# Kernel tuning notes

Hardware: AMD Instinct MI355X
Metric: run time of the kernel (lower is better)

## Reference

```python
import jax, jax.numpy as jnp
import numpy as np

TIMESTEPS = 1000


def setup_inputs() -> dict:
    key = jax.random.key(0)
    k1, k2 = jax.random.split(key)
    rec = jax.random.uniform(k1, (64, 1, 256, 256), dtype=jnp.float32)
    tgt = jax.random.uniform(k2, (64, 1, 256, 256), dtype=jnp.float32)
    return {"reconstructed_image": rec, "target_image": tgt}


def _holographic_transform(img):
    # img: [B, 1, H, W] -> out: [B, 1, H, TIMESTEPS]
    # Original: for every nonzero pixel (x, y) with value v, writes
    #   out[b, 0, x, int(v * timesteps) - 1] = y
    # iterating in row-major (y ascending) order, so for duplicate targets the
    B, C, H, W = img.shape
    x = img[:, 0]  # [B, H, W]
    q = (x * TIMESTEPS).astype(jnp.int32) - 1
    # torch negative indexing wraps (q = -1 -> timesteps - 1); zero pixels are
    # skipped, so route them to an out-of-range index and drop.
    q = jnp.where(x != 0, q % TIMESTEPS, TIMESTEPS)  # [B, H, W]
    y_vals = jnp.broadcast_to(jnp.arange(W, dtype=img.dtype), (B, H, W))
    b_idx = jnp.arange(B)[:, None, None]
    h_idx = jnp.arange(H)[None, :, None]
    out = jnp.zeros((B, 1, H, TIMESTEPS), dtype=img.dtype)
    out = out.at[b_idx, 0, h_idx, q].max(y_vals, mode="drop")
    return out


def reference(reconstructed_image, target_image):
    rec_holo = _holographic_transform(reconstructed_image)
    tgt_holo = _holographic_transform(target_image)
    return jnp.mean((rec_holo - tgt_holo) ** 2)
```

## Files before the change

### kernel.cpp

```cpp
#include <hip/hip_runtime.h>

#define TIMESTEPS 1000
#define NROWS 16384
#define ROWS_PER_WAVE 4
#define WAVES_PER_BLOCK 4
#define NBLOCKS (NROWS / (ROWS_PER_WAVE * WAVES_PER_BLOCK))
#define NPARTIALS (NROWS / ROWS_PER_WAVE)
#define TOTAL_ELEMS 16384000.0

__global__ __launch_bounds__(256) void holo_row_loss(
    const float* __restrict__ rec,
    const float* __restrict__ tgt,
    float* __restrict__ partials)
{
    __shared__ int bins[WAVES_PER_BLOCK][2048];

    const int tid  = threadIdx.x;
    const int wav  = tid >> 6;
    const int lane = tid & 63;
    const int gw   = blockIdx.x * WAVES_PER_BLOCK + wav;

    int* __restrict__ binw = &bins[wav][0];

    int4 z4; z4.x = 0; z4.y = 0; z4.z = 0; z4.w = 0;
    int4* zb = (int4*)binw;
#pragma unroll
    for (int j = 0; j < 8; ++j) zb[j * 64 + lane] = z4;
    __builtin_amdgcn_wave_barrier();

    const float4* rec4 = (const float4*)rec;
    const float4* tgt4 = (const float4*)tgt;

    float s = 0.0f;

#pragma unroll 1
    for (int r = 0; r < ROWS_PER_WAVE; ++r) {
        const int row = gw * ROWS_PER_WAVE + r;
        const float4 xr = rec4[row * 64 + lane];
        const float4 xt = tgt4[row * 64 + lane];

        int qr[4], qt[4];
#pragma unroll
        for (int j = 0; j < 4; ++j) {
            const float vr = (&xr.x)[j];
            const float vt = (&xt.x)[j];
            const int   w  = lane * 4 + j;
            int q = (int)(vr * 1000.0f) - 1;
            if (q < 0) q += TIMESTEPS;
            if (vr != 0.0f) { atomicMax(&binw[q], w); qr[j] = q; }
            else            { qr[j] = 1012; }
            q = (int)(vt * 1000.0f) - 1;
            if (q < 0) q += TIMESTEPS;
            if (vt != 0.0f) { atomicMax(&binw[1024 + q], w); qt[j] = q; }
            else            { qt[j] = 1012; }
        }
        __builtin_amdgcn_wave_barrier();

        const int4* r4 = (const int4*)binw;
        const int4* t4 = (const int4*)(binw + 1024);
#pragma unroll
        for (int k = 0; k < 4; ++k) {
            const int4 a = r4[k * 64 + lane];
            const int4 b = t4[k * 64 + lane];
            const float d0 = (float)(a.x - b.x);
            const float d1 = (float)(a.y - b.y);
            const float d2 = (float)(a.z - b.z);
            const float d3 = (float)(a.w - b.w);
            s = fmaf(d0, d0, s);
            s = fmaf(d1, d1, s);
            s = fmaf(d2, d2, s);
            s = fmaf(d3, d3, s);
        }
        __builtin_amdgcn_wave_barrier();

#pragma unroll
        for (int j = 0; j < 4; ++j) {
            binw[qr[j]] = 0;
            binw[1024 + qt[j]] = 0;
        }
        __builtin_amdgcn_wave_barrier();
    }

    for (int off = 32; off > 0; off >>= 1) s += __shfl_down(s, off, 64);
    if (lane == 0) partials[gw] = s;
}

__global__ __launch_bounds__(256) void reduce_partials(
    const float* __restrict__ partials,
    float* __restrict__ out)
{
    __shared__ double wave_sums[4];
    const int tid = threadIdx.x;
    double s = 0.0;
#pragma unroll
    for (int i = 0; i < NPARTIALS / 256; ++i)
        s += (double)partials[i * 256 + tid];
    for (int off = 32; off > 0; off >>= 1) s += __shfl_down(s, off, 64);
    if ((tid & 63) == 0) wave_sums[tid >> 6] = s;
    __syncthreads();
    if (tid == 0) {
        double tot = wave_sums[0] + wave_sums[1] + wave_sums[2] + wave_sums[3];
        out[0] = (float)(tot / TOTAL_ELEMS);
    }
}

extern "C" void kernel_launch(void* const* d_in, const int* in_sizes, int n_in,
                              void* d_out, int out_size, void* d_ws, size_t ws_size,
                              hipStream_t stream)
{
    const float* rec = (const float*)d_in[0];
    const float* tgt = (const float*)d_in[1];
    float* out = (float*)d_out;
    float* partials = (float*)d_ws;

    holo_row_loss<<<NBLOCKS, 256, 0, stream>>>(rec, tgt, partials);
    reduce_partials<<<1, 256, 0, stream>>>(partials, out);
}
```

Measured before the change: 75.99 us.

## Process each image row with a full block instead of one wave

Restructures the per-row histogram so all 256 threads of a block handle one 256-pixel row, with one pixel per thread and a single shared bin array. All 8 rows' inputs are prefetched into registers up front, and bins are cleared by reading and zeroing in the same pass. Accumulation switches to exact integer arithmetic, producing 2048 integer partials. The cost is two block-wide __syncthreads per row in place of wave barriers, and integer sums could overflow if differences grow large.

```diff
diff --git a/kernel.cpp b/kernel.cpp
--- a/kernel.cpp
+++ b/kernel.cpp
@@ -2,99 +2,81 @@
 
 #define TIMESTEPS 1000
 #define NROWS 16384
-#define ROWS_PER_WAVE 4
-#define WAVES_PER_BLOCK 4
-#define NBLOCKS (NROWS / (ROWS_PER_WAVE * WAVES_PER_BLOCK))
-#define NPARTIALS (NROWS / ROWS_PER_WAVE)
+#define ROWS_PER_BLOCK 8
+#define NBLOCKS (NROWS / ROWS_PER_BLOCK)
 #define TOTAL_ELEMS 16384000.0
 
-__global__ __launch_bounds__(256) void holo_row_loss(
+__global__ __launch_bounds__(256, 8) void holo_block_loss(
     const float* __restrict__ rec,
     const float* __restrict__ tgt,
-    float* __restrict__ partials)
+    int* __restrict__ partials)
 {
-    __shared__ int bins[WAVES_PER_BLOCK][2048];
+    __shared__ __align__(16) int bins[2048];
+    __shared__ int wsum[4];
 
     const int tid  = threadIdx.x;
-    const int wav  = tid >> 6;
-    const int lane = tid & 63;
-    const int gw   = blockIdx.x * WAVES_PER_BLOCK + wav;
+    const int base = blockIdx.x * (ROWS_PER_BLOCK * 256) + tid;
 
-    int* __restrict__ binw = &bins[wav][0];
+    float rv[ROWS_PER_BLOCK], tv[ROWS_PER_BLOCK];
+#pragma unroll
+    for (int r = 0; r < ROWS_PER_BLOCK; ++r) {
+        rv[r] = rec[base + r * 256];
+        tv[r] = tgt[base + r * 256];
+    }
 
     int4 z4; z4.x = 0; z4.y = 0; z4.z = 0; z4.w = 0;
-    int4* zb = (int4*)binw;
-#pragma unroll
-    for (int j = 0; j < 8; ++j) zb[j * 64 + lane] = z4;
-    __builtin_amdgcn_wave_barrier();
+    int4* zb = (int4*)bins;
+    zb[tid]       = z4;
+    zb[256 + tid] = z4;
 
-    const float4* rec4 = (const float4*)rec;
-    const float4* tgt4 = (const float4*)tgt;
-
-    float s = 0.0f;
-
-#pragma unroll 1
-    for (int r = 0; r < ROWS_PER_WAVE; ++r) {
-        const int row = gw * ROWS_PER_WAVE + r;
-        const float4 xr = rec4[row * 64 + lane];
-        const float4 xt = tgt4[row * 64 + lane];
-
-        int qr[4], qt[4];
-#pragma unroll
-        for (int j = 0; j < 4; ++j) {
-            const float vr = (&xr.x)[j];
-            const float vt = (&xt.x)[j];
-            const int   w  = lane * 4 + j;
-            int q = (int)(vr * 1000.0f) - 1;
-            if (q < 0) q += TIMESTEPS;
-            if (vr != 0.0f) { atomicMax(&binw[q], w); qr[j] = q; }
-            else            { qr[j] = 1012; }
-            q = (int)(vt * 1000.0f) - 1;
-            if (q < 0) q += TIMESTEPS;
-            if (vt != 0.0f) { atomicMax(&binw[1024 + q], w); qt[j] = q; }
-            else            { qt[j] = 1012; }
-        }
-        __builtin_amdgcn_wave_barrier();
-
-        const int4* r4 = (const int4*)binw;
-        const int4* t4 = (const int4*)(binw + 1024);
-#pragma unroll
-        for (int k = 0; k < 4; ++k) {
-            const int4 a = r4[k * 64 + lane];
-            const int4 b = t4[k * 64 + lane];
-            const float d0 = (float)(a.x - b.x);
-            const float d1 = (float)(a.y - b.y);
-            const float d2 = (float)(a.z - b.z);
-            const float d3 = (float)(a.w - b.w);
-            s = fmaf(d0, d0, s);
-            s = fmaf(d1, d1, s);
-            s = fmaf(d2, d2, s);
-            s = fmaf(d3, d3, s);
-        }
-        __builtin_amdgcn_wave_barrier();
+    int s = 0;
+    __syncthreads();
 
 #pragma unroll
-        for (int j = 0; j < 4; ++j) {
-            binw[qr[j]] = 0;
-            binw[1024 + qt[j]] = 0;
-        }
-        __builtin_amdgcn_wave_barrier();
+    for (int r = 0; r < ROWS_PER_BLOCK; ++r) {
+        const float vr = rv[r];
+        const float vt = tv[r];
+        int q = (int)(vr * 1000.0f) - 1;
+        if (q < 0) q += TIMESTEPS;
+        if (vr != 0.0f) atomicMax(&bins[q], tid);
+        q = (int)(vt * 1000.0f) - 1;
+        if (q < 0) q += TIMESTEPS;
+        if (vt != 0.0f) atomicMax(&bins[1024 + q], tid);
+        __syncthreads();
+
+        const int4 a = ((const int4*)bins)[tid];
+        const int4 b = ((const int4*)bins)[256 + tid];
+        zb[tid]       = z4;
+        zb[256 + tid] = z4;
+        int d;
+        d = a.x - b.x; s += d * d;
+        d = a.y - b.y; s += d * d;
+        d = a.z - b.z; s += d * d;
+        d = a.w - b.w; s += d * d;
+        __syncthreads();
     }
 
     for (int off = 32; off > 0; off >>= 1) s += __shfl_down(s, off, 64);
-    if (lane == 0) partials[gw] = s;
+    if ((tid & 63) == 0) wsum[tid >> 6] = s;
+    __syncthreads();
+    if (tid == 0)
+        partials[blockIdx.x] = wsum[0] + wsum[1] + wsum[2] + wsum[3];
 }
 
 __global__ __launch_bounds__(256) void reduce_partials(
-    const float* __restrict__ partials,
+    const int* __restrict__ partials,
     float* __restrict__ out)
 {
     __shared__ double wave_sums[4];
     const int tid = threadIdx.x;
+    const int4* p4 = (const int4*)partials;
+    const int4 u = p4[tid & 255];
+    const int4 v = p4[256 + (tid & 255)];
     double s = 0.0;
-#pragma unroll
-    for (int i = 0; i < NPARTIALS / 256; ++i)
-        s += (double)partials[i * 256 + tid];
+    if (tid < 256) {
+        s = (double)u.x + (double)u.y + (double)u.z + (double)u.w
+          + (double)v.x + (double)v.y + (double)v.z + (double)v.w;
+    }
     for (int off = 32; off > 0; off >>= 1) s += __shfl_down(s, off, 64);
     if ((tid & 63) == 0) wave_sums[tid >> 6] = s;
     __syncthreads();
@@ -111,8 +93,8 @@
     const float* rec = (const float*)d_in[0];
     const float* tgt = (const float*)d_in[1];
     float* out = (float*)d_out;
-    float* partials = (float*)d_ws;
+    int* partials = (int*)d_ws;
 
-    holo_row_loss<<<NBLOCKS, 256, 0, stream>>>(rec, tgt, partials);
+    holo_block_loss<<<NBLOCKS, 256, 0, stream>>>(rec, tgt, partials);
     reduce_partials<<<1, 256, 0, stream>>>(partials, out);
 }
```

Result: slower. 77.96 us (+2.6%).
